# Optimization experiments

Hardware: AMD Instinct MI355X
Metric: run time of the kernel (lower is better)

Reference implementation:

```python
import jax, jax.numpy as jnp
import numpy as np

DT_RANK = 64
D_STATE = 16


def setup_inputs() -> dict:
    key = jax.random.key(0)
    ks = jax.random.split(key, 6)
    B, L, Di = 2, 2048, 2048
    x = jax.random.normal(ks[0], (B, L, Di), dtype=jnp.float32)
    W_xproj = jax.random.normal(ks[1], (DT_RANK + 2 * D_STATE, Di), dtype=jnp.float32) * (Di ** -0.5)
    W_dt = jax.random.uniform(ks[2], (Di, DT_RANK), dtype=jnp.float32, minval=-(DT_RANK ** -0.5), maxval=DT_RANK ** -0.5)
    dt = jnp.exp(jax.random.uniform(ks[3], (Di,), dtype=jnp.float32) * (np.log(0.1) - np.log(0.001)) + np.log(0.001))
    b_dt = dt + jnp.log(-jnp.expm1(-dt))
    A_log = jnp.log(jnp.broadcast_to(jnp.arange(1, D_STATE + 1, dtype=jnp.float32), (Di, D_STATE)))
    D_param = jnp.ones((Di,), dtype=jnp.float32)
    return {"x": x, "W_xproj": W_xproj, "W_dt": W_dt, "b_dt": b_dt, "A_log": A_log, "D_param": D_param}


def _selective_scan(u, delta, A, Bm, Cm):
    # u, delta: (b, l, d); A: (d, n); Bm, Cm: (b, l, n)
    deltaA = jnp.exp(delta[..., None] * A[None, None])          # (b, l, d, n)
    deltaB_u = delta[..., None] * Bm[:, :, None, :] * u[..., None]  # (b, l, d, n)

    def step(h, inp):
        dA, dBu, c = inp                      # dA,dBu: (b,d,n); c: (b,n)
        h = dA * h + dBu
        y = jnp.einsum('bdn,bn->bd', h, c)
        return h, y

    b, l, d = u.shape
    h0 = jnp.zeros((b, d, A.shape[1]), dtype=u.dtype)
    xs = (jnp.moveaxis(deltaA, 1, 0), jnp.moveaxis(deltaB_u, 1, 0), jnp.moveaxis(Cm, 1, 0))
    _, ys = jax.lax.scan(step, h0, xs)        # ys: (l, b, d)
    return jnp.moveaxis(ys, 0, 1)


def reference(x, W_xproj, W_dt, b_dt, A_log, D_param):
    x_dbl = jnp.einsum('bld,ed->ble', x, W_xproj)  # (b, l, dt_rank + 2*n)
    dlt = x_dbl[..., :DT_RANK]
    Bm = x_dbl[..., DT_RANK:DT_RANK + D_STATE]
    Cm = x_dbl[..., DT_RANK + D_STATE:]
    delta = jax.nn.softplus(jnp.einsum('blr,dr->bld', dlt, W_dt) + b_dt)
    A = -jnp.exp(A_log.astype(jnp.float32))
    y = _selective_scan(x, delta, A, Bm, Cm)
    return y + x * D_param[None, None, :]
```

## Files before the change

### kernel.cpp

```cpp
#include <hip/hip_runtime.h>

#define BATCH 2
#define L_SEQ 2048
#define DI 2048
#define NROW (BATCH * L_SEQ)
#define E_DIM 96
#define RNK 64
#define NST 16
#define NCH 32
#define CL 32
#define SPLITK 16
#define KSL (DI / SPLITK)

#define WS_XDBL 0
#define WS_PART 393216
#define WS_HLOC 393216
#define WS_DSUM (393216 + 2097152)
#define WS_HENT (393216 + 6291456)
#define WS_WDTT (WS_HENT + 2097152)

__device__ __forceinline__ float softplusf(float z) {
    return fmaxf(z, 0.f) + __logf(1.f + __expf(-fabsf(z)));
}

__device__ __forceinline__ void barrier_lds() {
    asm volatile("s_waitcnt lgkmcnt(0)" ::: "memory");
    __builtin_amdgcn_s_barrier();
}

#define PCHAIN_E16(DCV) \
    float p1 = __expf((DCV) * A0); \
    float p2 = p1 * p1, p3 = p2 * p1, p4 = p2 * p2, p5 = p4 * p1; \
    float p6 = p3 * p3, p7 = p4 * p3, p8 = p4 * p4; \
    float e_[16] = {p1, p2, p3, p4, p5, p6, p7, p8, \
                    p8 * p1, p5 * p5, p8 * p3, p6 * p6, \
                    p8 * p5, p7 * p7, p8 * p7, p8 * p8};

__global__ __launch_bounds__(512) void gemm_xproj_part(const float* __restrict__ x,
                                                       const float* __restrict__ Wx,
                                                       float* __restrict__ part) {
    __shared__ float xs[32][132];
    __shared__ float wsh[32][100];
    const int tid = threadIdx.x;
    const int r0 = blockIdx.x * 128;
    const int kbase0 = blockIdx.y * KSL;
    const int rg = tid >> 4;
    const int cg = tid & 15;

    float acc[4][6];
#pragma unroll
    for (int i = 0; i < 4; i++)
#pragma unroll
        for (int j = 0; j < 6; j++) acc[i][j] = 0.f;

    for (int kt = 0; kt < KSL / 32; kt++) {
        const int kb = kbase0 + kt * 32;
#pragma unroll
        for (int rep = 0; rep < 2; rep++) {
            int i = rep * 512 + tid;
            int row = i >> 3, kq = i & 7;
            float4 v = *(const float4*)&x[(long)(r0 + row) * DI + kb + kq * 4];
            xs[kq * 4 + 0][row] = v.x;
            xs[kq * 4 + 1][row] = v.y;
            xs[kq * 4 + 2][row] = v.z;
            xs[kq * 4 + 3][row] = v.w;
        }
        {
            int e = tid >> 3, kq = tid & 7;
            float4 v = *(const float4*)&Wx[(long)e * DI + kb + kq * 4];
            wsh[kq * 4 + 0][e] = v.x;
            wsh[kq * 4 + 1][e] = v.y;
            wsh[kq * 4 + 2][e] = v.z;
            wsh[kq * 4 + 3][e] = v.w;
        }
        if (tid < 256) {
            int i = 512 + tid;
            int e = i >> 3, kq = i & 7;
            float4 v = *(const float4*)&Wx[(long)e * DI + kb + kq * 4];
            wsh[kq * 4 + 0][e] = v.x;
            wsh[kq * 4 + 1][e] = v.y;
            wsh[kq * 4 + 2][e] = v.z;
            wsh[kq * 4 + 3][e] = v.w;
        }
        __syncthreads();
#pragma unroll 8
        for (int k = 0; k < 32; k++) {
            float4 xa = *(const float4*)&xs[k][rg * 4];
            float xr[4] = {xa.x, xa.y, xa.z, xa.w};
            float wr[6];
#pragma unroll
            for (int j = 0; j < 6; j++) wr[j] = wsh[k][cg * 6 + j];
#pragma unroll
            for (int i = 0; i < 4; i++)
#pragma unroll
                for (int j = 0; j < 6; j++) acc[i][j] = fmaf(xr[i], wr[j], acc[i][j]);
        }
        __syncthreads();
    }
    const long sbase = (long)blockIdx.y * NROW * E_DIM;
#pragma unroll
    for (int i = 0; i < 4; i++) {
        long rowb = sbase + (long)(r0 + rg * 4 + i) * E_DIM + cg * 6;
#pragma unroll
        for (int j = 0; j < 6; j++) part[rowb + j] = acc[i][j];
    }
}

__global__ __launch_bounds__(256) void xproj_reduce_wt(const float* __restrict__ part,
                                                       float* __restrict__ xdbl,
                                                       const float* __restrict__ Wdt,
                                                       float* __restrict__ wdtT) {
    if (blockIdx.x < 384) {
        const int i4 = blockIdx.x * 256 + threadIdx.x;
        const float4* p4 = (const float4*)part;
        float4 s = p4[i4];
#pragma unroll
        for (int sp = 1; sp < SPLITK; sp++) {
            float4 v = p4[(long)sp * (NROW * E_DIM / 4) + i4];
            s.x += v.x; s.y += v.y; s.z += v.z; s.w += v.w;
        }
        ((float4*)xdbl)[i4] = s;
    } else {
        const int t = (blockIdx.x - 384) * 256 + threadIdx.x;
        const int base = t * 4;
        const int r = base >> 11;
        const int d4 = base & (DI - 1);
        float4 o;
        o.x = Wdt[(long)(d4 + 0) * RNK + r];
        o.y = Wdt[(long)(d4 + 1) * RNK + r];
        o.z = Wdt[(long)(d4 + 2) * RNK + r];
        o.w = Wdt[(long)(d4 + 3) * RNK + r];
        *(float4*)&wdtT[base] = o;
    }
}

#define PWT 256
#define PD 36
__global__ __launch_bounds__(256) void gemm_dt_scan(const float* __restrict__ x,
                                                    const float* __restrict__ xdbl,
                                                    const float* __restrict__ wdtT,
                                                    const float* __restrict__ b_dt,
                                                    const float* __restrict__ A_log,
                                                    float* __restrict__ delta,
                                                    float* __restrict__ hloc,
                                                    float* __restrict__ dsumb) {
    __shared__ float region[32 * PWT + 32 * PD];
    __shared__ float bsm[CL * NST];
    float* wt  = region;
    float* dlb = region + 32 * PWT;
    float* dtt = region;

    const int tid = threadIdx.x;
    const int d0 = blockIdx.x * 256;
    const int c = blockIdx.y;
    const int b = blockIdx.z;
    const int row0 = b * L_SEQ + c * 64;
    const int d = d0 + tid;
    const int rg = tid >> 6;
    const int cg = tid & 63;

    float h[16];
#pragma unroll
    for (int n = 0; n < 16; n++) h[n] = 0.f;
    float dsum = 0.f;
    float A0 = 0.f; bool fast = false;
    float4 bb;
    float xv[CL]; float4 bsv; float4 av[4];

#pragma unroll
    for (int s = 0; s < 2; s++) {
        const int rowS = row0 + s * CL;
        if (s) barrier_lds();
        float acc[8][4];
#pragma unroll
        for (int i = 0; i < 8; i++)
#pragma unroll
            for (int j = 0; j < 4; j++) acc[i][j] = 0.f;

#pragma unroll
        for (int kt = 0; kt < 2; kt++) {
            const int kb = kt * 32;
#pragma unroll
            for (int rep = 0; rep < 8; rep++) {
                int i = rep * 256 + tid;
                int k = i >> 6, c4 = i & 63;
                *(float4*)&wt[k * PWT + c4 * 4] =
                    *(const float4*)&wdtT[(long)(kb + k) * DI + d0 + c4 * 4];
            }
            {
                int r = tid >> 3, kq = tid & 7;
                float4 v = *(const float4*)&xdbl[(long)(rowS + r) * E_DIM + kb + kq * 4];
                dlb[(kq * 4 + 0) * PD + r] = v.x;
                dlb[(kq * 4 + 1) * PD + r] = v.y;
                dlb[(kq * 4 + 2) * PD + r] = v.z;
                dlb[(kq * 4 + 3) * PD + r] = v.w;
            }
            if (kt == 0) {
#pragma unroll
                for (int ll = 0; ll < CL; ll++)
                    xv[ll] = x[(long)(rowS + ll) * DI + d];
                if (tid < 128) {
                    int r = tid >> 2, q = tid & 3;
                    bsv = *(const float4*)&xdbl[(long)(rowS + r) * E_DIM + 64 + q * 4];
                }
                if (s == 0) {
#pragma unroll
                    for (int q = 0; q < 4; q++)
                        av[q] = *(const float4*)&A_log[(long)d * NST + q * 4];
                    bb = *(const float4*)&b_dt[d0 + cg * 4];
                }
            }
            barrier_lds();
#pragma unroll 8
            for (int k = 0; k < 32; k++) {
                float4 xa = *(const float4*)&dlb[k * PD + rg * 8];
                float4 xb = *(const float4*)&dlb[k * PD + rg * 8 + 4];
                float4 w4 = *(const float4*)&wt[k * PWT + cg * 4];
                float xr[8] = {xa.x, xa.y, xa.z, xa.w, xb.x, xb.y, xb.z, xb.w};
#pragma unroll
                for (int i = 0; i < 8; i++) {
                    acc[i][0] = fmaf(xr[i], w4.x, acc[i][0]);
                    acc[i][1] = fmaf(xr[i], w4.y, acc[i][1]);
                    acc[i][2] = fmaf(xr[i], w4.z, acc[i][2]);
                    acc[i][3] = fmaf(xr[i], w4.w, acc[i][3]);
                }
            }
            barrier_lds();
        }

#pragma unroll
        for (int i = 0; i < 8; i++) {
            int r = rg * 8 + i;
            float4 o;
            o.x = softplusf(acc[i][0] + bb.x);
            o.y = softplusf(acc[i][1] + bb.y);
            o.z = softplusf(acc[i][2] + bb.z);
            o.w = softplusf(acc[i][3] + bb.w);
            *(float4*)&delta[(long)(rowS + r) * DI + d0 + cg * 4] = o;
            *(float4*)&dtt[r * 256 + cg * 4] = o;
        }
        if (tid < 128) {
            int r = tid >> 2, q = tid & 3;
            *(float4*)&bsm[r * NST + q * 4] = bsv;
        }
        if (s == 0) {
            float a16[16];
#pragma unroll
            for (int q = 0; q < 4; q++) {
                a16[q * 4 + 0] = -__expf(av[q].x);
                a16[q * 4 + 1] = -__expf(av[q].y);
                a16[q * 4 + 2] = -__expf(av[q].z);
                a16[q * 4 + 3] = -__expf(av[q].w);
            }
            A0 = a16[0];
            fast = true;
#pragma unroll
            for (int n = 1; n < 16; n++)
                fast = fast && (fabsf(a16[n] - (float)(n + 1) * A0) <= 1e-4f * (float)(n + 1));
        }
        barrier_lds();

        if (fast) {
            for (int ll = 0; ll < CL; ll++) {
                float dc = dtt[ll * 256 + tid];
                float du = dc * xv[ll];
                PCHAIN_E16(dc);
#pragma unroll
                for (int q = 0; q < 4; q++) {
                    float4 v = *(const float4*)&bsm[ll * NST + q * 4];
                    h[q * 4 + 0] = fmaf(e_[q * 4 + 0], h[q * 4 + 0], du * v.x);
                    h[q * 4 + 1] = fmaf(e_[q * 4 + 1], h[q * 4 + 1], du * v.y);
                    h[q * 4 + 2] = fmaf(e_[q * 4 + 2], h[q * 4 + 2], du * v.z);
                    h[q * 4 + 3] = fmaf(e_[q * 4 + 3], h[q * 4 + 3], du * v.w);
                }
                dsum += dc;
            }
        } else {
            float Ag[16];
#pragma unroll
            for (int q = 0; q < 4; q++) {
                float4 t = *(const float4*)&A_log[(long)d * NST + q * 4];
                Ag[q * 4 + 0] = -__expf(t.x); Ag[q * 4 + 1] = -__expf(t.y);
                Ag[q * 4 + 2] = -__expf(t.z); Ag[q * 4 + 3] = -__expf(t.w);
            }
            for (int ll = 0; ll < CL; ll++) {
                float dc = dtt[ll * 256 + tid];
                float du = dc * xv[ll];
#pragma unroll
                for (int q = 0; q < 4; q++) {
                    float4 v = *(const float4*)&bsm[ll * NST + q * 4];
                    h[q * 4 + 0] = fmaf(__expf(dc * Ag[q * 4 + 0]), h[q * 4 + 0], du * v.x);
                    h[q * 4 + 1] = fmaf(__expf(dc * Ag[q * 4 + 1]), h[q * 4 + 1], du * v.y);
                    h[q * 4 + 2] = fmaf(__expf(dc * Ag[q * 4 + 2]), h[q * 4 + 2], du * v.z);
                    h[q * 4 + 3] = fmaf(__expf(dc * Ag[q * 4 + 3]), h[q * 4 + 3], du * v.w);
                }
                dsum += dc;
            }
        }
    }
    const long cb = (long)(b * NCH + c);
#pragma unroll
    for (int n = 0; n < 16; n++)
        hloc[(cb * NST + n) * DI + d] = h[n];
    dsumb[cb * DI + d] = dsum;
}

__global__ __launch_bounds__(256, 1) void scan_prefix(const float* __restrict__ A_log,
                                                      const float* __restrict__ hloc,
                                                      const float* __restrict__ dsumb,
                                                      float* __restrict__ hent) {
    const int gidx = blockIdx.x * 256 + threadIdx.x;
    const int d = gidx & (DI - 1);
    const int n = (gidx >> 11) & 15;
    const int b = gidx >> 15;
    const float An = -__expf(A_log[(long)d * NST + n]);
    float hl[NCH], dsv[NCH];
#pragma unroll
    for (int cc = 0; cc < NCH; cc++) {
        hl[cc]  = hloc[((long)(b * NCH + cc) * NST + n) * DI + d];
        dsv[cc] = dsumb[(long)(b * NCH + cc) * DI + d];
    }
    float e[NCH];
#pragma unroll
    for (int cc = 0; cc < NCH; cc++) e[cc] = __expf(An * dsv[cc]);
    float hc = 0.f;
#pragma unroll
    for (int cc = 0; cc < NCH; cc++) {
        hent[((long)(b * NCH + cc) * NST + n) * DI + d] = hc;
        hc = fmaf(e[cc], hc, hl[cc]);
    }
}

__global__ __launch_bounds__(256) void scan_out(const float* __restrict__ x,
                                                const float* __restrict__ xdbl,
                                                const float* __restrict__ A_log,
                                                const float* __restrict__ Dp,
                                                const float* __restrict__ hent,
                                                float* __restrict__ out) {
    __shared__ float bsm[64 * NST];
    __shared__ float csm[64 * NST];
    const int tid = threadIdx.x;
    const int d0 = blockIdx.x * 256;
    const int c = blockIdx.y;
    const int b = blockIdx.z;
    const int row0 = b * L_SEQ + c * 64;
    const int d = d0 + tid;

    {
        int r = tid >> 2, q = tid & 3;
        ((float4*)bsm)[tid] = *(const float4*)&xdbl[(long)(row0 + r) * E_DIM + 64 + q * 4];
        ((float4*)csm)[tid] = *(const float4*)&xdbl[(long)(row0 + r) * E_DIM + 80 + q * 4];
    }
    __syncthreads();

    float4 av[4];
#pragma unroll
    for (int q = 0; q < 4; q++)
        av[q] = *(const float4*)&A_log[(long)d * NST + q * 4];
    const long cb = (long)(b * NCH + c);
    float h[16];
#pragma unroll
    for (int n = 0; n < 16; n++)
        h[n] = hent[(cb * NST + n) * DI + d];
    const float Dd = Dp[d];

    float A[16];
#pragma unroll
    for (int q = 0; q < 4; q++) {
        A[q * 4 + 0] = -__expf(av[q].x);
        A[q * 4 + 1] = -__expf(av[q].y);
        A[q * 4 + 2] = -__expf(av[q].z);
        A[q * 4 + 3] = -__expf(av[q].w);
    }
    const float A0 = A[0];
    bool fast = true;
#pragma unroll
    for (int n = 1; n < 16; n++)
        fast = fast && (fabsf(A[n] - (float)(n + 1) * A0) <= 1e-4f * (float)(n + 1));

#pragma unroll
    for (int s = 0; s < 2; s++) {
        const int rowS = row0 + s * CL;
        float dv[CL], xvv[CL];
#pragma unroll
        for (int ll = 0; ll < CL; ll++) {
            dv[ll] = out[(long)(rowS + ll) * DI + d];
            xvv[ll] = x[(long)(rowS + ll) * DI + d];
        }
        long idx = (long)rowS * DI + d;
        if (fast) {
            for (int ll = 0; ll < CL; ll++) {
                float dc = dv[ll];
                float xc = xvv[ll];
                float du = dc * xc;
                PCHAIN_E16(dc);
                float y = 0.f;
#pragma unroll
                for (int q = 0; q < 4; q++) {
                    float4 v = *(const float4*)&bsm[(s * CL + ll) * NST + q * 4];
                    float4 w = *(const float4*)&csm[(s * CL + ll) * NST + q * 4];
                    h[q * 4 + 0] = fmaf(e_[q * 4 + 0], h[q * 4 + 0], du * v.x);
                    h[q * 4 + 1] = fmaf(e_[q * 4 + 1], h[q * 4 + 1], du * v.y);
                    h[q * 4 + 2] = fmaf(e_[q * 4 + 2], h[q * 4 + 2], du * v.z);
                    h[q * 4 + 3] = fmaf(e_[q * 4 + 3], h[q * 4 + 3], du * v.w);
                    y = fmaf(h[q * 4 + 0], w.x, y);
                    y = fmaf(h[q * 4 + 1], w.y, y);
                    y = fmaf(h[q * 4 + 2], w.z, y);
                    y = fmaf(h[q * 4 + 3], w.w, y);
                }
                out[idx] = fmaf(xc, Dd, y);
                idx += DI;
            }
        } else {
            for (int ll = 0; ll < CL; ll++) {
                float dc = dv[ll];
                float xc = xvv[ll];
                float du = dc * xc;
                float y = 0.f;
#pragma unroll
                for (int q = 0; q < 4; q++) {
                    float4 v = *(const float4*)&bsm[(s * CL + ll) * NST + q * 4];
                    float4 w = *(const float4*)&csm[(s * CL + ll) * NST + q * 4];
                    h[q * 4 + 0] = fmaf(__expf(dc * A[q * 4 + 0]), h[q * 4 + 0], du * v.x);
                    h[q * 4 + 1] = fmaf(__expf(dc * A[q * 4 + 1]), h[q * 4 + 1], du * v.y);
                    h[q * 4 + 2] = fmaf(__expf(dc * A[q * 4 + 2]), h[q * 4 + 2], du * v.z);
                    h[q * 4 + 3] = fmaf(__expf(dc * A[q * 4 + 3]), h[q * 4 + 3], du * v.w);
                    y = fmaf(h[q * 4 + 0], w.x, y);
                    y = fmaf(h[q * 4 + 1], w.y, y);
                    y = fmaf(h[q * 4 + 2], w.z, y);
                    y = fmaf(h[q * 4 + 3], w.w, y);
                }
                out[idx] = fmaf(xc, Dd, y);
                idx += DI;
            }
        }
    }
}

extern "C" void kernel_launch(void* const* d_in, const int* in_sizes, int n_in,
                              void* d_out, int out_size, void* d_ws, size_t ws_size,
                              hipStream_t stream) {
    const float* x    = (const float*)d_in[0];
    const float* Wx   = (const float*)d_in[1];
    const float* Wdt  = (const float*)d_in[2];
    const float* bdt  = (const float*)d_in[3];
    const float* Alog = (const float*)d_in[4];
    const float* Dp   = (const float*)d_in[5];
    float* out = (float*)d_out;
    float* ws = (float*)d_ws;
    float* xdbl  = ws + WS_XDBL;
    float* partb = ws + WS_PART;
    float* hloc  = ws + WS_HLOC;
    float* dsumb = ws + WS_DSUM;
    float* hent  = ws + WS_HENT;
    float* wdtT  = ws + WS_WDTT;

    gemm_xproj_part<<<dim3(NROW / 128, SPLITK), 512, 0, stream>>>(x, Wx, partb);
    xproj_reduce_wt<<<dim3(512), 256, 0, stream>>>(partb, xdbl, Wdt, wdtT);
    gemm_dt_scan<<<dim3(DI / 256, NCH, BATCH), 256, 0, stream>>>(x, xdbl, wdtT, bdt, Alog,
                                                                 out, hloc, dsumb);
    scan_prefix<<<dim3(BATCH * DI * NST / 256), 256, 0, stream>>>(Alog, hloc, dsumb, hent);
    scan_out<<<dim3(DI / 256, NCH, BATCH), 256, 0, stream>>>(x, xdbl, Alog, Dp, hent, out);
}
```

Measured before the change: 208.8 us.

## Halve scan chunk length to double chunk-level parallelism and prefetch weight tiles

Doubles the number of sequence chunks, so each block of the delta-GEMM-plus-local-scan and final-output kernels handles 32 rows instead of 64. The goal is twice as many blocks for better occupancy and a shorter serial scan per block. In exchange, the cross-chunk carry kernel now walks a serial chain of 64 chunks, which it software-pipelines with 8-wide prefetches. The workspace offsets are reshuffled so the hloc and dsum buffers hold the doubled chunk count. The GEMM kernel prefetches the second K-tile of W_dt and delta into registers while the first tile is computed, and pads the LDS row stride to 260 to reduce bank conflicts.

```diff
diff --git a/kernel.cpp b/kernel.cpp
--- a/kernel.cpp
+++ b/kernel.cpp
@@ -7,7 +7,7 @@
 #define E_DIM 96
 #define RNK 64
 #define NST 16
-#define NCH 32
+#define NCH 64
 #define CL 32
 #define SPLITK 16
 #define KSL (DI / SPLITK)
@@ -15,9 +15,9 @@
 #define WS_XDBL 0
 #define WS_PART 393216
 #define WS_HLOC 393216
-#define WS_DSUM (393216 + 2097152)
+#define WS_DSUM (393216 + 4194304)
 #define WS_HENT (393216 + 6291456)
-#define WS_WDTT (WS_HENT + 2097152)
+#define WS_WDTT (393216 + 6291456)
 
 __device__ __forceinline__ float softplusf(float z) {
     return fmaxf(z, 0.f) + __logf(1.f + __expf(-fabsf(z)));
@@ -134,7 +134,7 @@
     }
 }
 
-#define PWT 256
+#define PW 260
 #define PD 36
 __global__ __launch_bounds__(256) void gemm_dt_scan(const float* __restrict__ x,
                                                     const float* __restrict__ xdbl,
@@ -144,158 +144,173 @@
                                                     float* __restrict__ delta,
                                                     float* __restrict__ hloc,
                                                     float* __restrict__ dsumb) {
-    __shared__ float region[32 * PWT + 32 * PD];
+    __shared__ float region[32 * PW + 32 * PD];
     __shared__ float bsm[CL * NST];
     float* wt  = region;
-    float* dlb = region + 32 * PWT;
+    float* dlb = region + 32 * PW;
     float* dtt = region;
 
     const int tid = threadIdx.x;
     const int d0 = blockIdx.x * 256;
     const int c = blockIdx.y;
     const int b = blockIdx.z;
-    const int row0 = b * L_SEQ + c * 64;
+    const int row0 = b * L_SEQ + c * CL;
     const int d = d0 + tid;
     const int rg = tid >> 6;
     const int cg = tid & 63;
 
+    if (tid < 128) {
+        int r = tid >> 2, q = tid & 3;
+        ((float4*)bsm)[tid] = *(const float4*)&xdbl[(long)(row0 + r) * E_DIM + 64 + q * 4];
+    }
+
+    float acc[8][4];
+#pragma unroll
+    for (int i = 0; i < 8; i++)
+#pragma unroll
+        for (int j = 0; j < 4; j++) acc[i][j] = 0.f;
+
+#pragma unroll
+    for (int rep = 0; rep < 8; rep++) {
+        int i = rep * 256 + tid;
+        int k = i >> 6, c4 = i & 63;
+        *(float4*)&wt[k * PW + c4 * 4] =
+            *(const float4*)&wdtT[(long)k * DI + d0 + c4 * 4];
+    }
+    {
+        int r = tid >> 3, kq = tid & 7;
+        float4 v = *(const float4*)&xdbl[(long)(row0 + r) * E_DIM + kq * 4];
+        dlb[(kq * 4 + 0) * PD + r] = v.x;
+        dlb[(kq * 4 + 1) * PD + r] = v.y;
+        dlb[(kq * 4 + 2) * PD + r] = v.z;
+        dlb[(kq * 4 + 3) * PD + r] = v.w;
+    }
+    float4 wq[8];
+#pragma unroll
+    for (int rep = 0; rep < 8; rep++) {
+        int i = rep * 256 + tid;
+        int k = i >> 6, c4 = i & 63;
+        wq[rep] = *(const float4*)&wdtT[(long)(32 + k) * DI + d0 + c4 * 4];
+    }
+    float4 dq;
+    { int r = tid >> 3, kq = tid & 7;
+      dq = *(const float4*)&xdbl[(long)(row0 + r) * E_DIM + 32 + kq * 4]; }
+
+    barrier_lds();
+#pragma unroll 8
+    for (int k = 0; k < 32; k++) {
+        float4 xa = *(const float4*)&dlb[k * PD + rg * 8];
+        float4 xb = *(const float4*)&dlb[k * PD + rg * 8 + 4];
+        float4 w4 = *(const float4*)&wt[k * PW + cg * 4];
+        float xr[8] = {xa.x, xa.y, xa.z, xa.w, xb.x, xb.y, xb.z, xb.w};
+#pragma unroll
+        for (int i = 0; i < 8; i++) {
+            acc[i][0] = fmaf(xr[i], w4.x, acc[i][0]);
+            acc[i][1] = fmaf(xr[i], w4.y, acc[i][1]);
+            acc[i][2] = fmaf(xr[i], w4.z, acc[i][2]);
+            acc[i][3] = fmaf(xr[i], w4.w, acc[i][3]);
+        }
+    }
+    barrier_lds();
+#pragma unroll
+    for (int rep = 0; rep < 8; rep++) {
+        int i = rep * 256 + tid;
+        int k = i >> 6, c4 = i & 63;
+        *(float4*)&wt[k * PW + c4 * 4] = wq[rep];
+    }
+    {
+        int r = tid >> 3, kq = tid & 7;
+        dlb[(kq * 4 + 0) * PD + r] = dq.x;
+        dlb[(kq * 4 + 1) * PD + r] = dq.y;
+        dlb[(kq * 4 + 2) * PD + r] = dq.z;
+        dlb[(kq * 4 + 3) * PD + r] = dq.w;
+    }
+    float xv[CL];
+#pragma unroll
+    for (int ll = 0; ll < CL; ll++)
+        xv[ll] = x[(long)(row0 + ll) * DI + d];
+    float4 av[4];
+#pragma unroll
+    for (int q = 0; q < 4; q++)
+        av[q] = *(const float4*)&A_log[(long)d * NST + q * 4];
+    float4 bb = *(const float4*)&b_dt[d0 + cg * 4];
+
+    barrier_lds();
+#pragma unroll 8
+    for (int k = 0; k < 32; k++) {
+        float4 xa = *(const float4*)&dlb[k * PD + rg * 8];
+        float4 xb = *(const float4*)&dlb[k * PD + rg * 8 + 4];
+        float4 w4 = *(const float4*)&wt[k * PW + cg * 4];
+        float xr[8] = {xa.x, xa.y, xa.z, xa.w, xb.x, xb.y, xb.z, xb.w};
+#pragma unroll
+        for (int i = 0; i < 8; i++) {
+            acc[i][0] = fmaf(xr[i], w4.x, acc[i][0]);
+            acc[i][1] = fmaf(xr[i], w4.y, acc[i][1]);
+            acc[i][2] = fmaf(xr[i], w4.z, acc[i][2]);
+            acc[i][3] = fmaf(xr[i], w4.w, acc[i][3]);
+        }
+    }
+    barrier_lds();
+
+#pragma unroll
+    for (int i = 0; i < 8; i++) {
+        int r = rg * 8 + i;
+        float4 o;
+        o.x = softplusf(acc[i][0] + bb.x);
+        o.y = softplusf(acc[i][1] + bb.y);
+        o.z = softplusf(acc[i][2] + bb.z);
+        o.w = softplusf(acc[i][3] + bb.w);
+        *(float4*)&delta[(long)(row0 + r) * DI + d0 + cg * 4] = o;
+        *(float4*)&dtt[r * 256 + cg * 4] = o;
+    }
+
+    float A[16];
+#pragma unroll
+    for (int q = 0; q < 4; q++) {
+        A[q * 4 + 0] = -__expf(av[q].x);
+        A[q * 4 + 1] = -__expf(av[q].y);
+        A[q * 4 + 2] = -__expf(av[q].z);
+        A[q * 4 + 3] = -__expf(av[q].w);
+    }
+    const float A0 = A[0];
+    bool fast = true;
+#pragma unroll
+    for (int n = 1; n < 16; n++)
+        fast = fast && (fabsf(A[n] - (float)(n + 1) * A0) <= 1e-4f * (float)(n + 1));
+    barrier_lds();
+
     float h[16];
 #pragma unroll
     for (int n = 0; n < 16; n++) h[n] = 0.f;
     float dsum = 0.f;
-    float A0 = 0.f; bool fast = false;
-    float4 bb;
-    float xv[CL]; float4 bsv; float4 av[4];
-
-#pragma unroll
-    for (int s = 0; s < 2; s++) {
-        const int rowS = row0 + s * CL;
-        if (s) barrier_lds();
-        float acc[8][4];
-#pragma unroll
-        for (int i = 0; i < 8; i++)
-#pragma unroll
-            for (int j = 0; j < 4; j++) acc[i][j] = 0.f;
-
-#pragma unroll
-        for (int kt = 0; kt < 2; kt++) {
-            const int kb = kt * 32;
-#pragma unroll
-            for (int rep = 0; rep < 8; rep++) {
-                int i = rep * 256 + tid;
-                int k = i >> 6, c4 = i & 63;
-                *(float4*)&wt[k * PWT + c4 * 4] =
-                    *(const float4*)&wdtT[(long)(kb + k) * DI + d0 + c4 * 4];
+    if (fast) {
+        for (int ll = 0; ll < CL; ll++) {
+            float dc = dtt[ll * 256 + tid];
+            float du = dc * xv[ll];
+            PCHAIN_E16(dc);
+#pragma unroll
+            for (int q = 0; q < 4; q++) {
+                float4 v = *(const float4*)&bsm[ll * NST + q * 4];
+                h[q * 4 + 0] = fmaf(e_[q * 4 + 0], h[q * 4 + 0], du * v.x);
+                h[q * 4 + 1] = fmaf(e_[q * 4 + 1], h[q * 4 + 1], du * v.y);
+                h[q * 4 + 2] = fmaf(e_[q * 4 + 2], h[q * 4 + 2], du * v.z);
+                h[q * 4 + 3] = fmaf(e_[q * 4 + 3], h[q * 4 + 3], du * v.w);
             }
-            {
-                int r = tid >> 3, kq = tid & 7;
-                float4 v = *(const float4*)&xdbl[(long)(rowS + r) * E_DIM + kb + kq * 4];
-                dlb[(kq * 4 + 0) * PD + r] = v.x;
-                dlb[(kq * 4 + 1) * PD + r] = v.y;
-                dlb[(kq * 4 + 2) * PD + r] = v.z;
-                dlb[(kq * 4 + 3) * PD + r] = v.w;
+            dsum += dc;
+        }
+    } else {
+        for (int ll = 0; ll < CL; ll++) {
+            float dc = dtt[ll * 256 + tid];
+            float du = dc * xv[ll];
+#pragma unroll
+            for (int q = 0; q < 4; q++) {
+                float4 v = *(const float4*)&bsm[ll * NST + q * 4];
+                h[q * 4 + 0] = fmaf(__expf(dc * A[q * 4 + 0]), h[q * 4 + 0], du * v.x);
+                h[q * 4 + 1] = fmaf(__expf(dc * A[q * 4 + 1]), h[q * 4 + 1], du * v.y);
+                h[q * 4 + 2] = fmaf(__expf(dc * A[q * 4 + 2]), h[q * 4 + 2], du * v.z);
+                h[q * 4 + 3] = fmaf(__expf(dc * A[q * 4 + 3]), h[q * 4 + 3], du * v.w);
             }
-            if (kt == 0) {
-#pragma unroll
-                for (int ll = 0; ll < CL; ll++)
-                    xv[ll] = x[(long)(rowS + ll) * DI + d];
-                if (tid < 128) {
-                    int r = tid >> 2, q = tid & 3;
-                    bsv = *(const float4*)&xdbl[(long)(rowS + r) * E_DIM + 64 + q * 4];
-                }
-                if (s == 0) {
-#pragma unroll
-                    for (int q = 0; q < 4; q++)
-                        av[q] = *(const float4*)&A_log[(long)d * NST + q * 4];
-                    bb = *(const float4*)&b_dt[d0 + cg * 4];
-                }
-            }
-            barrier_lds();
-#pragma unroll 8
-            for (int k = 0; k < 32; k++) {
-                float4 xa = *(const float4*)&dlb[k * PD + rg * 8];
-                float4 xb = *(const float4*)&dlb[k * PD + rg * 8 + 4];
-                float4 w4 = *(const float4*)&wt[k * PWT + cg * 4];
-                float xr[8] = {xa.x, xa.y, xa.z, xa.w, xb.x, xb.y, xb.z, xb.w};
-#pragma unroll
-                for (int i = 0; i < 8; i++) {
-                    acc[i][0] = fmaf(xr[i], w4.x, acc[i][0]);
-                    acc[i][1] = fmaf(xr[i], w4.y, acc[i][1]);
-                    acc[i][2] = fmaf(xr[i], w4.z, acc[i][2]);
-                    acc[i][3] = fmaf(xr[i], w4.w, acc[i][3]);
-                }
-            }
-            barrier_lds();
-        }
-
-#pragma unroll
-        for (int i = 0; i < 8; i++) {
-            int r = rg * 8 + i;
-            float4 o;
-            o.x = softplusf(acc[i][0] + bb.x);
-            o.y = softplusf(acc[i][1] + bb.y);
-            o.z = softplusf(acc[i][2] + bb.z);
-            o.w = softplusf(acc[i][3] + bb.w);
-            *(float4*)&delta[(long)(rowS + r) * DI + d0 + cg * 4] = o;
-            *(float4*)&dtt[r * 256 + cg * 4] = o;
-        }
-        if (tid < 128) {
-            int r = tid >> 2, q = tid & 3;
-            *(float4*)&bsm[r * NST + q * 4] = bsv;
-        }
-        if (s == 0) {
-            float a16[16];
-#pragma unroll
-            for (int q = 0; q < 4; q++) {
-                a16[q * 4 + 0] = -__expf(av[q].x);
-                a16[q * 4 + 1] = -__expf(av[q].y);
-                a16[q * 4 + 2] = -__expf(av[q].z);
-                a16[q * 4 + 3] = -__expf(av[q].w);
-            }
-            A0 = a16[0];
-            fast = true;
-#pragma unroll
-            for (int n = 1; n < 16; n++)
-                fast = fast && (fabsf(a16[n] - (float)(n + 1) * A0) <= 1e-4f * (float)(n + 1));
-        }
-        barrier_lds();
-
-        if (fast) {
-            for (int ll = 0; ll < CL; ll++) {
-                float dc = dtt[ll * 256 + tid];
-                float du = dc * xv[ll];
-                PCHAIN_E16(dc);
-#pragma unroll
-                for (int q = 0; q < 4; q++) {
-                    float4 v = *(const float4*)&bsm[ll * NST + q * 4];
-                    h[q * 4 + 0] = fmaf(e_[q * 4 + 0], h[q * 4 + 0], du * v.x);
-                    h[q * 4 + 1] = fmaf(e_[q * 4 + 1], h[q * 4 + 1], du * v.y);
-                    h[q * 4 + 2] = fmaf(e_[q * 4 + 2], h[q * 4 + 2], du * v.z);
-                    h[q * 4 + 3] = fmaf(e_[q * 4 + 3], h[q * 4 + 3], du * v.w);
-                }
-                dsum += dc;
-            }
-        } else {
-            float Ag[16];
-#pragma unroll
-            for (int q = 0; q < 4; q++) {
-                float4 t = *(const float4*)&A_log[(long)d * NST + q * 4];
-                Ag[q * 4 + 0] = -__expf(t.x); Ag[q * 4 + 1] = -__expf(t.y);
-                Ag[q * 4 + 2] = -__expf(t.z); Ag[q * 4 + 3] = -__expf(t.w);
-            }
-            for (int ll = 0; ll < CL; ll++) {
-                float dc = dtt[ll * 256 + tid];
-                float du = dc * xv[ll];
-#pragma unroll
-                for (int q = 0; q < 4; q++) {
-                    float4 v = *(const float4*)&bsm[ll * NST + q * 4];
-                    h[q * 4 + 0] = fmaf(__expf(dc * Ag[q * 4 + 0]), h[q * 4 + 0], du * v.x);
-                    h[q * 4 + 1] = fmaf(__expf(dc * Ag[q * 4 + 1]), h[q * 4 + 1], du * v.y);
-                    h[q * 4 + 2] = fmaf(__expf(dc * Ag[q * 4 + 2]), h[q * 4 + 2], du * v.z);
-                    h[q * 4 + 3] = fmaf(__expf(dc * Ag[q * 4 + 3]), h[q * 4 + 3], du * v.w);
-                }
-                dsum += dc;
-            }
+            dsum += dc;
         }
     }
     const long cb = (long)(b * NCH + c);
@@ -314,20 +329,33 @@
     const int n = (gidx >> 11) & 15;
     const int b = gidx >> 15;
     const float An = -__expf(A_log[(long)d * NST + n]);
-    float hl[NCH], dsv[NCH];
-#pragma unroll
-    for (int cc = 0; cc < NCH; cc++) {
-        hl[cc]  = hloc[((long)(b * NCH + cc) * NST + n) * DI + d];
-        dsv[cc] = dsumb[(long)(b * NCH + cc) * DI + d];
-    }
-    float e[NCH];
-#pragma unroll
-    for (int cc = 0; cc < NCH; cc++) e[cc] = __expf(An * dsv[cc]);
+    const long hstr = (long)NST * DI;
+    const long hbase = (long)b * NCH * hstr + (long)n * DI + d;
+    const long dbase = (long)b * NCH * DI + d;
+
+    float hl[8], ds8[8], hln[8], dsn[8];
+#pragma unroll
+    for (int j = 0; j < 8; j++) {
+        hl[j]  = hloc[hbase + j * hstr];
+        ds8[j] = dsumb[dbase + j * DI];
+    }
     float hc = 0.f;
 #pragma unroll
-    for (int cc = 0; cc < NCH; cc++) {
-        hent[((long)(b * NCH + cc) * NST + n) * DI + d] = hc;
-        hc = fmaf(e[cc], hc, hl[cc]);
+    for (int c8 = 0; c8 < NCH; c8 += 8) {
+        if (c8 + 8 < NCH) {
+#pragma unroll
+            for (int j = 0; j < 8; j++) {
+                hln[j] = hloc[hbase + (c8 + 8 + j) * hstr];
+                dsn[j] = dsumb[dbase + (c8 + 8 + j) * DI];
+            }
+        }
+#pragma unroll
+        for (int j = 0; j < 8; j++) {
+            hent[hbase + (c8 + j) * hstr] = hc;
+            hc = fmaf(__expf(An * ds8[j]), hc, hl[j]);
+        }
+#pragma unroll
+        for (int j = 0; j < 8; j++) { hl[j] = hln[j]; ds8[j] = dsn[j]; }
     }
 }
 
@@ -337,19 +365,20 @@
                                                 const float* __restrict__ Dp,
                                                 const float* __restrict__ hent,
                                                 float* __restrict__ out) {
-    __shared__ float bsm[64 * NST];
-    __shared__ float csm[64 * NST];
+    __shared__ float bsm[CL * NST];
+    __shared__ float csm[CL * NST];
     const int tid = threadIdx.x;
     const int d0 = blockIdx.x * 256;
     const int c = blockIdx.y;
     const int b = blockIdx.z;
-    const int row0 = b * L_SEQ + c * 64;
+    const int row0 = b * L_SEQ + c * CL;
     const int d = d0 + tid;
 
     {
-        int r = tid >> 2, q = tid & 3;
-        ((float4*)bsm)[tid] = *(const float4*)&xdbl[(long)(row0 + r) * E_DIM + 64 + q * 4];
-        ((float4*)csm)[tid] = *(const float4*)&xdbl[(long)(row0 + r) * E_DIM + 80 + q * 4];
+        int i = tid & 127, r = i >> 2, q = i & 3;
+        float4 v = *(const float4*)&xdbl[(long)(row0 + r) * E_DIM + 64 + ((tid >> 7) << 4) + q * 4];
+        if (tid < 128) ((float4*)bsm)[i] = v;
+        else           ((float4*)csm)[i] = v;
     }
     __syncthreads();
 
@@ -358,11 +387,18 @@
     for (int q = 0; q < 4; q++)
         av[q] = *(const float4*)&A_log[(long)d * NST + q * 4];
     const long cb = (long)(b * NCH + c);
-    float h[16];
+    float hv[16];
 #pragma unroll
     for (int n = 0; n < 16; n++)
-        h[n] = hent[(cb * NST + n) * DI + d];
+        hv[n] = hent[(cb * NST + n) * DI + d];
     const float Dd = Dp[d];
+
+    float dv[CL], xvv[CL];
+#pragma unroll
+    for (int ll = 0; ll < CL; ll++) {
+        dv[ll] = out[(long)(row0 + ll) * DI + d];
+        xvv[ll] = x[(long)(row0 + ll) * DI + d];
+    }
 
     float A[16];
 #pragma unroll
@@ -377,62 +413,55 @@
 #pragma unroll
     for (int n = 1; n < 16; n++)
         fast = fast && (fabsf(A[n] - (float)(n + 1) * A0) <= 1e-4f * (float)(n + 1));
-
-#pragma unroll
-    for (int s = 0; s < 2; s++) {
-        const int rowS = row0 + s * CL;
-        float dv[CL], xvv[CL];
-#pragma unroll
+    float h[16];
+#pragma unroll
+    for (int n = 0; n < 16; n++) h[n] = hv[n];
+
+    long idx = (long)row0 * DI + d;
+    if (fast) {
         for (int ll = 0; ll < CL; ll++) {
-            dv[ll] = out[(long)(rowS + ll) * DI + d];
-            xvv[ll] = x[(long)(rowS + ll) * DI + d];
-        }
-        long idx = (long)rowS * DI + d;
-        if (fast) {
-            for (int ll = 0; ll < CL; ll++) {
-                float dc = dv[ll];
-                float xc = xvv[ll];
-                float du = dc * xc;
-                PCHAIN_E16(dc);
-                float y = 0.f;
-#pragma unroll
-                for (int q = 0; q < 4; q++) {
-                    float4 v = *(const float4*)&bsm[(s * CL + ll) * NST + q * 4];
-                    float4 w = *(const float4*)&csm[(s * CL + ll) * NST + q * 4];
-                    h[q * 4 + 0] = fmaf(e_[q * 4 + 0], h[q * 4 + 0], du * v.x);
-                    h[q * 4 + 1] = fmaf(e_[q * 4 + 1], h[q * 4 + 1], du * v.y);
-                    h[q * 4 + 2] = fmaf(e_[q * 4 + 2], h[q * 4 + 2], du * v.z);
-                    h[q * 4 + 3] = fmaf(e_[q * 4 + 3], h[q * 4 + 3], du * v.w);
-                    y = fmaf(h[q * 4 + 0], w.x, y);
-                    y = fmaf(h[q * 4 + 1], w.y, y);
-                    y = fmaf(h[q * 4 + 2], w.z, y);
-                    y = fmaf(h[q * 4 + 3], w.w, y);
-                }
-                out[idx] = fmaf(xc, Dd, y);
-                idx += DI;
+            float dc = dv[ll];
+            float xc = xvv[ll];
+            float du = dc * xc;
+            PCHAIN_E16(dc);
+            float y = 0.f;
+#pragma unroll
+            for (int q = 0; q < 4; q++) {
+                float4 v = *(const float4*)&bsm[ll * NST + q * 4];
+                float4 w = *(const float4*)&csm[ll * NST + q * 4];
+                h[q * 4 + 0] = fmaf(e_[q * 4 + 0], h[q * 4 + 0], du * v.x);
+                h[q * 4 + 1] = fmaf(e_[q * 4 + 1], h[q * 4 + 1], du * v.y);
+                h[q * 4 + 2] = fmaf(e_[q * 4 + 2], h[q * 4 + 2], du * v.z);
+                h[q * 4 + 3] = fmaf(e_[q * 4 + 3], h[q * 4 + 3], du * v.w);
+                y = fmaf(h[q * 4 + 0], w.x, y);
+                y = fmaf(h[q * 4 + 1], w.y, y);
+                y = fmaf(h[q * 4 + 2], w.z, y);
+                y = fmaf(h[q * 4 + 3], w.w, y);
             }
-        } else {
-            for (int ll = 0; ll < CL; ll++) {
-                float dc = dv[ll];
-                float xc = xvv[ll];
-                float du = dc * xc;
-                float y = 0.f;
-#pragma unroll
-                for (int q = 0; q < 4; q++) {
-                    float4 v = *(const float4*)&bsm[(s * CL + ll) * NST + q * 4];
-                    float4 w = *(const float4*)&csm[(s * CL + ll) * NST + q * 4];
-                    h[q * 4 + 0] = fmaf(__expf(dc * A[q * 4 + 0]), h[q * 4 + 0], du * v.x);
-                    h[q * 4 + 1] = fmaf(__expf(dc * A[q * 4 + 1]), h[q * 4 + 1], du * v.y);
-                    h[q * 4 + 2] = fmaf(__expf(dc * A[q * 4 + 2]), h[q * 4 + 2], du * v.z);
-                    h[q * 4 + 3] = fmaf(__expf(dc * A[q * 4 + 3]), h[q * 4 + 3], du * v.w);
-                    y = fmaf(h[q * 4 + 0], w.x, y);
-                    y = fmaf(h[q * 4 + 1], w.y, y);
-                    y = fmaf(h[q * 4 + 2], w.z, y);
-                    y = fmaf(h[q * 4 + 3], w.w, y);
-                }
-                out[idx] = fmaf(xc, Dd, y);
-                idx += DI;
+            out[idx] = fmaf(xc, Dd, y);
+            idx += DI;
+        }
+    } else {
+        for (int ll = 0; ll < CL; ll++) {
+            float dc = dv[ll];
+            float xc = xvv[ll];
+            float du = dc * xc;
+            float y = 0.f;
+#pragma unroll
+            for (int q = 0; q < 4; q++) {
+                float4 v = *(const float4*)&bsm[ll * NST + q * 4];
+                float4 w = *(const float4*)&csm[ll * NST + q * 4];
+                h[q * 4 + 0] = fmaf(__expf(dc * A[q * 4 + 0]), h[q * 4 + 0], du * v.x);
+                h[q * 4 + 1] = fmaf(__expf(dc * A[q * 4 + 1]), h[q * 4 + 1], du * v.y);
+                h[q * 4 + 2] = fmaf(__expf(dc * A[q * 4 + 2]), h[q * 4 + 2], du * v.z);
+                h[q * 4 + 3] = fmaf(__expf(dc * A[q * 4 + 3]), h[q * 4 + 3], du * v.w);
+                y = fmaf(h[q * 4 + 0], w.x, y);
+                y = fmaf(h[q * 4 + 1], w.y, y);
+                y = fmaf(h[q * 4 + 2], w.z, y);
+                y = fmaf(h[q * 4 + 3], w.w, y);
             }
+            out[idx] = fmaf(xc, Dd, y);
+            idx += DI;
         }
     }
 }
```

After: 185.2 us (median of 2 runs). 1.13x faster.
